# Performance work log

Hardware: AMD Instinct MI355X
Metric: run time of the kernel (lower is better)

Reference implementation:

```python
import jax, jax.numpy as jnp
import numpy as np
from jax.scipy.special import gammaln

# Problem sizes (static)
N = 50000          # nodes
P = 200000         # paths (source->target pairs in the transitive closure)
L = 6              # edges (nodes) per path -> flat edge list length E = P*L
E = P * L
MAX_DELAY = 128
DT = 1.0
T = int(MAX_DELAY * int(1 / DT))   # expanded time window (== 128)
EPS = 1e-12


def gamma_irf(params):
    """IRF_FN entry: per-node gamma (Nash-cascade) impulse response, [N, T]."""
    a = jax.nn.softplus(params[:, 0]) + 1.0      # shape  > 1
    b = jax.nn.softplus(params[:, 1]) + 0.5      # scale  > 0.5
    t = (jnp.arange(T, dtype=jnp.float32) + 0.5) * jnp.float32(DT)  # [T]
    log_irf = ((a[:, None] - 1.0) * jnp.log(t)[None, :]
               - t[None, :] / b[:, None]
               - gammaln(a)[:, None]
               - a[:, None] * jnp.log(b)[:, None])
    return jnp.exp(log_irf) * jnp.float32(DT)    # [N, T]


def setup_inputs() -> dict:
    key = jax.random.key(0)
    k1, k2 = jax.random.split(key)
    params = jax.random.normal(k1, (N, 2), dtype=jnp.float32)
    edges_flat = jax.random.randint(k2, (E,), 0, N, dtype=jnp.int32)
    path_cumsum = jnp.arange(P + 1, dtype=jnp.int32) * L  # segment offsets into edges_flat
    return {"params": params, "edges_flat": edges_flat, "path_cumsum": path_cumsum}


def reference(params, edges_flat, path_cumsum):
    # --- irf_fn + rfft ---------------------------------------------------
    irfs = gamma_irf(params)                          # [N, T]
    irfs_freq = jnp.fft.rfft(irfs, n=T, axis=-1)      # [N, F] complex64

    # --- log_transitive_closure: product of per-edge spectra along paths -
    log_f = jnp.log(irfs_freq + EPS)                  # complex log, [N, F]
    seg_ids = jnp.searchsorted(path_cumsum[1:], jnp.arange(E, dtype=path_cumsum.dtype),
                               side="right")          # [E] path id per flat edge
    path_log = jax.ops.segment_sum(log_f[edges_flat], seg_ids, num_segments=P)  # [P, F]
    path_freq = jnp.exp(path_log)                     # product along path, [P, F]

    # coords: (source node, target node) of each path; include_index_diag appends (i, i)
    src = edges_flat[path_cumsum[:-1]]
    dst = edges_flat[path_cumsum[1:] - 1]
    diag = jnp.arange(N, dtype=edges_flat.dtype)
    coords = jnp.stack([jnp.concatenate([src, diag]),
                        jnp.concatenate([dst, diag])])              # [2, P+N]
    freq_all = jnp.concatenate([path_freq, irfs_freq], axis=0)      # [P+N, F]

    # --- irfft + postprocessing ------------------------------------------
    irfs_agg = jnp.fft.irfft(freq_all, n=T, axis=-1)  # [P+N, T]
    irfs_agg = jax.nn.relu(irfs_agg)
    # sampler.phi_k: avg-pool by factor int(1/dt) == 1 -> identity when dt=1
    irfs_agg = jnp.flip(irfs_agg, axis=-1)
    irfs_agg = irfs_agg / (jnp.sum(irfs_agg, axis=-1, keepdims=True) + EPS)
    # SparseKernel(coords, values, kernel_size=(N, N, T)) -> return its contents
    return (coords, irfs_agg)
```

## Files before the change

### kernel.cpp

```cpp
#include <hip/hip_runtime.h>
#include <hip/hip_bf16.h>

#define N_NODES 50000
#define P_PATHS 200000
#define N_ROWS  250000
#define L_EDGES 6
#define T_LEN   128
#define F_BINS  65
#define EPSF    1e-12f
#define PIF     3.14159265358979323846f
#define COORD_ELEMS ((size_t)2 * (P_PATHS + N_NODES))
#define FREQ_BYTES  ((size_t)N_NODES * F_BINS * 8)
#define ATILE_OFF   ((size_t)32 * 1024 * 1024)
#define XTAB_OFF    ((size_t)96 * 1024 * 1024)
#define PCON_OFF    ((size_t)112 * 1024 * 1024)
#define KDIM  128
#define KPADN 128
#define ROWS_BLK 64
#define PATH_TILES (P_PATHS / ROWS_BLK)
#define TILES ((N_ROWS + ROWS_BLK - 1) / ROWS_BLK)
#define GEMM_GRID 1024
#define STILES ((N_NODES + ROWS_BLK - 1) / ROWS_BLK)

typedef _Float16 v2h __attribute__((ext_vector_type(2)));
typedef _Float16 v8h __attribute__((ext_vector_type(8)));
typedef float    v4f __attribute__((ext_vector_type(4)));

__device__ __forceinline__ float softplus_(float x) {
    const float e = __expf(-fabsf(x));
    return fmaxf(x, 0.0f) + __logf(1.0f + e);
}

__device__ __forceinline__ float lgamma_pos_(float x) {
    const float ser = 1.000000000190015f
                    + 76.18009172947146f     / (x + 1.0f)
                    - 86.50532032941677f     / (x + 2.0f)
                    + 24.01409824083091f     / (x + 3.0f)
                    - 1.231739572450155f     / (x + 4.0f)
                    + 0.1208650973866179e-2f / (x + 5.0f)
                    - 0.5395239384953e-5f    / (x + 6.0f);
    const float tmp = x + 5.5f;
    return (x + 0.5f) * __logf(tmp) - tmp + __logf(2.5066282746310005f * ser / x);
}

__global__ __launch_bounds__(256) void irfa49x_setup(const float* __restrict__ params,
                                                     _Float16* __restrict__ Wt,
                                                     _Float16* __restrict__ W2t,
                                                     float4* __restrict__ pcons) {
    const int b = blockIdx.x;
    if (b < 64) {
        const int idx = b * 256 + threadIdx.x;
        const int t  = idx >> 7;
        const int kk = idx & 127;
        int j; float cj; bool is_sin;
        if (kk == 1) { j = 64; cj = 1.0f; is_sin = false; }
        else {
            j = kk >> 1;
            cj = (j == 0) ? 1.0f : 2.0f;
            is_sin = (kk & 1);
        }
        const int m = (j * t) & 127;
        const float th = (float)m * (PIF / 64.0f);
        const float tri = is_sin ? -__sinf(th) : __cosf(th);
        Wt[idx] = (_Float16)(cj * tri * (1.0f / 128.0f));
    } else if (b < 128) {
        const int idx = (b - 64) * 256 + threadIdx.x;
        const int kk = idx >> 7;
        const int t  = idx & 127;
        int j; bool is_sin;
        if (kk == 1) { j = 64; is_sin = false; }
        else { j = kk >> 1; is_sin = (kk & 1); }
        const int m = (j * t) & 127;
        const float th = (float)m * (PIF / 64.0f);
        W2t[idx] = (_Float16)(is_sin ? -__sinf(th) : __cosf(th));
    } else {
        const int n = (b - 128) * 256 + threadIdx.x;
        if (n >= N_NODES) return;
        const float a  = softplus_(params[2 * n + 0]) + 1.0f;
        const float bb = softplus_(params[2 * n + 1]) + 0.5f;
        const float lg = lgamma_pos_(a);
        const float lb = __logf(bb);
        float4 pc;
        pc.x = a - 1.0f;
        pc.y = 1.0f / bb;
        pc.z = -lg - a * lb;
        pc.w = 0.0f;
        pcons[n] = pc;
    }
}

__global__ __launch_bounds__(256) void irfa49w_xgen(const float4* __restrict__ pcons,
                                                    _Float16* __restrict__ xtab) {
    const int tid  = threadIdx.x;
    const int node = blockIdx.x * 2 + (tid >> 7);
    const int t    = tid & 127;
    const float4 pc = pcons[node];
    const float tc = (float)t + 0.5f;
    const float x  = __expf(fmaf(pc.x, __logf(tc), fmaf(-tc, pc.y, pc.z)));
    xtab[(size_t)node * T_LEN + t] = (_Float16)x;
}

__global__ __launch_bounds__(256, 2) void irfa49x_spec(const _Float16* __restrict__ xtab,
                                                       const _Float16* __restrict__ W2t,
                                                       _Float16* __restrict__ freqh) {
    const int tid  = threadIdx.x;
    const int wv   = tid >> 6;
    const int lane = tid & 63;
    const int tcol = lane & 15;
    const int kg   = lane >> 4;
    const int rgrp = kg * 4;
    const int tile = blockIdx.x;

    v8h bf[4][8];
    #pragma unroll
    for (int kt = 0; kt < 4; ++kt) {
        #pragma unroll
        for (int nt = 0; nt < 8; ++nt) {
            bf[kt][nt] = *(const v8h*)&W2t[(nt * 16 + tcol) * 128 + kt * 32 + kg * 8];
        }
    }

    const int rowa = tile * ROWS_BLK + wv * 16 + tcol;
    v8h af[4];
    #pragma unroll
    for (int kt = 0; kt < 4; ++kt) {
        v8h v = (v8h){(_Float16)0.0f, (_Float16)0.0f, (_Float16)0.0f, (_Float16)0.0f,
                      (_Float16)0.0f, (_Float16)0.0f, (_Float16)0.0f, (_Float16)0.0f};
        if (rowa < N_NODES) v = *(const v8h*)&xtab[(size_t)rowa * T_LEN + kt * 32 + kg * 8];
        af[kt] = v;
    }

    v4f acc[8];
    #pragma unroll
    for (int nt = 0; nt < 8; ++nt) acc[nt] = (v4f){0.0f, 0.0f, 0.0f, 0.0f};
    #pragma unroll
    for (int kt = 0; kt < 4; ++kt) {
        #pragma unroll
        for (int nt = 0; nt < 8; ++nt) {
            acc[nt] = __builtin_amdgcn_mfma_f32_16x16x32_f16(af[kt], bf[kt][nt], acc[nt], 0, 0, 0);
        }
    }

    #pragma unroll
    for (int reg = 0; reg < 4; ++reg) {
        const int row = tile * ROWS_BLK + wv * 16 + rgrp + reg;
        if (row < N_NODES) {
            _Float16* op = freqh + (size_t)row * KPADN;
            #pragma unroll
            for (int nt = 0; nt < 8; ++nt) {
                op[nt * 16 + tcol] = (_Float16)acc[nt][reg];
            }
        }
    }
}

__global__ __launch_bounds__(256) void irfa49x_prod(const _Float16* __restrict__ freqh,
                                                    const int* __restrict__ edges,
                                                    _Float16* __restrict__ Atile) {
    const int gt  = blockIdx.x * 256 + threadIdx.x;
    const int row = gt >> 5;
    const int tl  = gt & 31;
    _Float16* op = Atile + (size_t)row * KDIM;

    const int eb = row * L_EDGES;
    v2h av[L_EDGES], bv[L_EDGES];
    #pragma unroll
    for (int j = 0; j < L_EDGES; ++j) {
        const _Float16* fh = freqh + (size_t)edges[eb + j] * KPADN;
        av[j] = *(const v2h*)(fh + 2 * tl);
        bv[j] = *(const v2h*)(fh + 64 + 2 * tl);
    }
    float p1r = 1.0f, p1i = 0.0f, p2r = 1.0f, p2i = 0.0f, q = 1.0f;
    #pragma unroll
    for (int j = 0; j < L_EDGES; ++j) {
        const float ax  = (float)av[j][0];
        const float ayr = (float)av[j][1];
        const float ay  = (tl == 0) ? 0.0f : ayr;
        float t1 = p1r * ax - p1i * ay;
        p1i      = p1r * ay + p1i * ax;
        p1r = t1;
        q *= ayr;
        const float bx = (float)bv[j][0], by = (float)bv[j][1];
        float t2 = p2r * bx - p2i * by;
        p2i      = p2r * by + p2i * bx;
        p2r = t2;
    }
    v2h h;
    h[0] = (_Float16)p1r;
    h[1] = (tl == 0) ? (_Float16)q : (_Float16)p1i;
    *(v2h*)(op + 2 * tl) = h;
    h[0] = (_Float16)p2r; h[1] = (_Float16)p2i;
    *(v2h*)(op + 64 + 2 * tl) = h;
}

__global__ __launch_bounds__(256, 2) void irfa49x_gemm(const _Float16* __restrict__ Atile,
                                                       const _Float16* __restrict__ freqh,
                                                       const _Float16* __restrict__ Wt,
                                                       float* __restrict__ out_agg) {
    const int tid  = threadIdx.x;
    const int wv   = tid >> 6;
    const int lane = tid & 63;
    const int tcol = lane & 15;
    const int kg   = lane >> 4;
    const int rgrp = kg * 4;

    v8h bf[4][8];
    #pragma unroll
    for (int kt = 0; kt < 4; ++kt) {
        #pragma unroll
        for (int nt = 0; nt < 8; ++nt) {
            bf[kt][nt] = *(const v8h*)&Wt[(nt * 16 + tcol) * KDIM + kt * 32 + kg * 8];
        }
    }

    for (int tile = blockIdx.x; tile < TILES; tile += GEMM_GRID) {
        const int rowa = tile * ROWS_BLK + wv * 16 + tcol;
        const _Float16* ap = (tile < PATH_TILES)
            ? Atile + (size_t)rowa * KDIM + kg * 8
            : freqh + (size_t)(rowa - P_PATHS) * KPADN + kg * 8;

        v8h af[4];
        #pragma unroll
        for (int kt = 0; kt < 4; ++kt) {
            v8h v = (v8h){(_Float16)0.0f, (_Float16)0.0f, (_Float16)0.0f, (_Float16)0.0f,
                          (_Float16)0.0f, (_Float16)0.0f, (_Float16)0.0f, (_Float16)0.0f};
            if (rowa < N_ROWS) v = *(const v8h*)(ap + kt * 32);
            af[kt] = v;
        }

        v4f acc[8];
        #pragma unroll
        for (int nt = 0; nt < 8; ++nt) acc[nt] = (v4f){0.0f, 0.0f, 0.0f, 0.0f};

        #pragma unroll
        for (int kt = 0; kt < 4; ++kt) {
            #pragma unroll
            for (int nt = 0; nt < 8; ++nt) {
                acc[nt] = __builtin_amdgcn_mfma_f32_16x16x32_f16(af[kt], bf[kt][nt], acc[nt], 0, 0, 0);
            }
        }

        #pragma unroll
        for (int reg = 0; reg < 4; ++reg) {
            float vals[8];
            float vsum = 0.0f;
            #pragma unroll
            for (int nt = 0; nt < 8; ++nt) {
                const float v = fmaxf(acc[nt][reg], 0.0f);
                vals[nt] = v;
                vsum += v;
            }
            vsum += __shfl_xor(vsum, 1);
            vsum += __shfl_xor(vsum, 2);
            vsum += __shfl_xor(vsum, 4);
            vsum += __shfl_xor(vsum, 8);
            const int row = tile * ROWS_BLK + wv * 16 + rgrp + reg;
            if (row < N_ROWS) {
                const float inv = 1.0f / (vsum + EPSF);
                float* op = out_agg + (size_t)row * T_LEN;
                #pragma unroll
                for (int nt = 0; nt < 8; ++nt) {
                    const int t = nt * 16 + tcol;
                    op[127 - t] = vals[nt] * inv;
                }
            }
        }
    }
}

__global__ void IRFAggregator_39049842655549_kernel(const int* __restrict__ edges,
                                                    float* __restrict__ out) {
    const int M = P_PATHS + N_NODES;
    const int i = blockIdx.x * blockDim.x + threadIdx.x;
    if (i >= 2 * M) return;
    int v;
    if (i < P_PATHS) {
        v = edges[i * L_EDGES];
    } else if (i < M) {
        v = i - P_PATHS;
    } else {
        const int j = i - M;
        if (j < P_PATHS) v = edges[j * L_EDGES + L_EDGES - 1];
        else             v = j - P_PATHS;
    }
    out[i] = (float)v;
}

extern "C" void kernel_launch(void* const* d_in, const int* in_sizes, int n_in,
                              void* d_out, int out_size, void* d_ws, size_t ws_size,
                              hipStream_t stream) {
    const float* params = (const float*)d_in[0];
    const int*   edges  = (const int*)d_in[1];

    _Float16* freqh = (_Float16*)d_ws;
    _Float16* Wt    = (_Float16*)((char*)d_ws + FREQ_BYTES);
    _Float16* W2t   = (_Float16*)((char*)d_ws + FREQ_BYTES + 65536);
    _Float16* Atile = (_Float16*)((char*)d_ws + ATILE_OFF);
    _Float16* xtab  = (_Float16*)((char*)d_ws + XTAB_OFF);
    float4*   pcons = (float4*)((char*)d_ws + PCON_OFF);
    float* out      = (float*)d_out;
    float* out_agg  = out + COORD_ELEMS;

    IRFAggregator_39049842655549_kernel<<<(int)((COORD_ELEMS + 255) / 256), 256, 0, stream>>>(edges, out);
    irfa49x_setup<<<128 + (N_NODES + 255) / 256, 256, 0, stream>>>(params, Wt, W2t, pcons);
    irfa49w_xgen<<<N_NODES / 2, 256, 0, stream>>>(pcons, xtab);
    irfa49x_spec<<<STILES, 256, 0, stream>>>(xtab, W2t, freqh);
    irfa49x_prod<<<(P_PATHS * 32) / 256, 256, 0, stream>>>(freqh, edges, Atile);
    irfa49x_gemm<<<GEMM_GRID, 256, 0, stream>>>(Atile, freqh, Wt, out_agg);
}
```

Measured before the change: 121.1 us.

## Stage GEMM output through LDS for vectorized reversed stores; widen prod loads

The GEMM epilogue now writes normalized, ReLU'd rows into a padded shared-memory tile. A second pass then emits them to global memory as float4 stores with the time reversal done in registers, replacing scattered scalar 4-byte stores. The path-product kernel now reads one 4-half vector per lane covering two adjacent bins, instead of two 2-half loads from separate halves of the row. It writes a matching 4-half output, so the K-layout stays consistent with the weight matrix. The cost is two extra block barriers per tile and 33 KB of LDS, which may affect occupancy.

```diff
diff --git a/kernel.cpp b/kernel.cpp
--- a/kernel.cpp
+++ b/kernel.cpp
@@ -21,8 +21,10 @@
 #define TILES ((N_ROWS + ROWS_BLK - 1) / ROWS_BLK)
 #define GEMM_GRID 1024
 #define STILES ((N_NODES + ROWS_BLK - 1) / ROWS_BLK)
+#define DPAD 132
 
 typedef _Float16 v2h __attribute__((ext_vector_type(2)));
+typedef _Float16 v4h __attribute__((ext_vector_type(4)));
 typedef _Float16 v8h __attribute__((ext_vector_type(8)));
 typedef float    v4f __attribute__((ext_vector_type(4)));
 
@@ -154,7 +156,7 @@
     }
 }
 
-__global__ __launch_bounds__(256) void irfa49x_prod(const _Float16* __restrict__ freqh,
+__global__ __launch_bounds__(256) void irfa49y_prod(const _Float16* __restrict__ freqh,
                                                     const int* __restrict__ edges,
                                                     _Float16* __restrict__ Atile) {
     const int gt  = blockIdx.x * 256 + threadIdx.x;
@@ -163,40 +165,39 @@
     _Float16* op = Atile + (size_t)row * KDIM;
 
     const int eb = row * L_EDGES;
-    v2h av[L_EDGES], bv[L_EDGES];
+    v4h fv[L_EDGES];
     #pragma unroll
     for (int j = 0; j < L_EDGES; ++j) {
-        const _Float16* fh = freqh + (size_t)edges[eb + j] * KPADN;
-        av[j] = *(const v2h*)(fh + 2 * tl);
-        bv[j] = *(const v2h*)(fh + 64 + 2 * tl);
-    }
-    float p1r = 1.0f, p1i = 0.0f, p2r = 1.0f, p2i = 0.0f, q = 1.0f;
+        fv[j] = *(const v4h*)(freqh + (size_t)edges[eb + j] * KPADN + 4 * tl);
+    }
+    float p0r = 1.0f, p0i = 0.0f, p1r = 1.0f, p1i = 0.0f, q = 1.0f;
     #pragma unroll
     for (int j = 0; j < L_EDGES; ++j) {
-        const float ax  = (float)av[j][0];
-        const float ayr = (float)av[j][1];
+        const float ax  = (float)fv[j][0];
+        const float ayr = (float)fv[j][1];
         const float ay  = (tl == 0) ? 0.0f : ayr;
-        float t1 = p1r * ax - p1i * ay;
-        p1i      = p1r * ay + p1i * ax;
-        p1r = t1;
+        float t1 = p0r * ax - p0i * ay;
+        p0i      = p0r * ay + p0i * ax;
+        p0r = t1;
         q *= ayr;
-        const float bx = (float)bv[j][0], by = (float)bv[j][1];
-        float t2 = p2r * bx - p2i * by;
-        p2i      = p2r * by + p2i * bx;
-        p2r = t2;
-    }
-    v2h h;
-    h[0] = (_Float16)p1r;
-    h[1] = (tl == 0) ? (_Float16)q : (_Float16)p1i;
-    *(v2h*)(op + 2 * tl) = h;
-    h[0] = (_Float16)p2r; h[1] = (_Float16)p2i;
-    *(v2h*)(op + 64 + 2 * tl) = h;
-}
-
-__global__ __launch_bounds__(256, 2) void irfa49x_gemm(const _Float16* __restrict__ Atile,
+        const float bx = (float)fv[j][2], by = (float)fv[j][3];
+        float t2 = p1r * bx - p1i * by;
+        p1i      = p1r * by + p1i * bx;
+        p1r = t2;
+    }
+    v4h h;
+    h[0] = (_Float16)p0r;
+    h[1] = (tl == 0) ? (_Float16)q : (_Float16)p0i;
+    h[2] = (_Float16)p1r;
+    h[3] = (_Float16)p1i;
+    *(v4h*)(op + 4 * tl) = h;
+}
+
+__global__ __launch_bounds__(256, 2) void irfa49y_gemm(const _Float16* __restrict__ Atile,
                                                        const _Float16* __restrict__ freqh,
                                                        const _Float16* __restrict__ Wt,
                                                        float* __restrict__ out_agg) {
+    __shared__ float sD[ROWS_BLK][DPAD];
     const int tid  = threadIdx.x;
     const int wv   = tid >> 6;
     const int lane = tid & 63;
@@ -213,6 +214,9 @@
         }
     }
 
+    const int srow = tid >> 2;
+    const int scb0 = (tid & 3) * 8;
+
     for (int tile = blockIdx.x; tile < TILES; tile += GEMM_GRID) {
         const int rowa = tile * ROWS_BLK + wv * 16 + tcol;
         const _Float16* ap = (tile < PATH_TILES)
@@ -254,17 +258,28 @@
             vsum += __shfl_xor(vsum, 2);
             vsum += __shfl_xor(vsum, 4);
             vsum += __shfl_xor(vsum, 8);
-            const int row = tile * ROWS_BLK + wv * 16 + rgrp + reg;
-            if (row < N_ROWS) {
-                const float inv = 1.0f / (vsum + EPSF);
-                float* op = out_agg + (size_t)row * T_LEN;
-                #pragma unroll
-                for (int nt = 0; nt < 8; ++nt) {
-                    const int t = nt * 16 + tcol;
-                    op[127 - t] = vals[nt] * inv;
-                }
-            }
-        }
+            const float inv = 1.0f / (vsum + EPSF);
+            const int drow = wv * 16 + rgrp + reg;
+            #pragma unroll
+            for (int nt = 0; nt < 8; ++nt) {
+                sD[drow][nt * 16 + tcol] = vals[nt] * inv;
+            }
+        }
+        __syncthreads();
+
+        const int grow = tile * ROWS_BLK + srow;
+        if (grow < N_ROWS) {
+            float* op = out_agg + (size_t)grow * T_LEN;
+            #pragma unroll
+            for (int c8 = 0; c8 < 8; ++c8) {
+                const int cb = scb0 + c8;
+                const float4 v = *(const float4*)&sD[srow][4 * cb];
+                float4 r;
+                r.x = v.w; r.y = v.z; r.z = v.y; r.w = v.x;
+                *(float4*)&op[124 - 4 * cb] = r;
+            }
+        }
+        __syncthreads();
     }
 }
 
@@ -305,6 +320,6 @@
     irfa49x_setup<<<128 + (N_NODES + 255) / 256, 256, 0, stream>>>(params, Wt, W2t, pcons);
     irfa49w_xgen<<<N_NODES / 2, 256, 0, stream>>>(pcons, xtab);
     irfa49x_spec<<<STILES, 256, 0, stream>>>(xtab, W2t, freqh);
-    irfa49x_prod<<<(P_PATHS * 32) / 256, 256, 0, stream>>>(freqh, edges, Atile);
-    irfa49x_gemm<<<GEMM_GRID, 256, 0, stream>>>(Atile, freqh, Wt, out_agg);
-}
+    irfa49y_prod<<<(P_PATHS * 32) / 256, 256, 0, stream>>>(freqh, edges, Atile);
+    irfa49y_gemm<<<GEMM_GRID, 256, 0, stream>>>(Atile, freqh, Wt, out_agg);
+}
```

Measured after the change: 140.5 us. 16.1% more time.
